# Performance work log

Measured on AMD Instinct MI355X. Metric: run time of the kernel, lower is better.

Reference implementation:

```python
import jax, jax.numpy as jnp
import numpy as np

N = 4096  # number of nodes (matches fill_max of edge indices)


def _dense(edges, n):
    # edges: [2, E] int; dense {0,1} adjacency. Duplicate edges collapse (set semantics).
    return jnp.zeros((n, n), dtype=jnp.float32).at[edges[0], edges[1]].set(1.0)


def setup_inputs() -> dict:
    key = jax.random.key(0)
    ks = jax.random.split(key, 4)
    E = 200000
    mk = lambda k: jax.random.randint(k, (2, E), 0, N, dtype=jnp.int32)
    return {
        "A_pos_t": mk(ks[0]),
        "A_pos_tp1": mk(ks[1]),
        "A_neg_t": mk(ks[2]),
        "A_neg_tp1": mk(ks[3]),
    }


def reference(A_pos_t, A_pos_tp1, A_neg_t, A_neg_tp1):
    p_t = _dense(A_pos_t, N)
    p1 = _dense(A_pos_tp1, N)
    n_t = _dense(A_neg_t, N)
    n1 = _dense(A_neg_tp1, N)

    # edge_index_diff: set symmetric difference == elementwise xor of {0,1} adjacency
    xor_p = p_t + p1 - 2.0 * p_t * p1
    xor_n = n_t + n1 - 2.0 * n_t * n1

    # Balance theory triangle closure on (tp1) graphs.
    # sign(a,b): +1 if pos edge (pos checked first -> priority), -1 elif neg edge.
    sp = p1                      # positive-sign edge indicator
    sn = n1 * (1.0 - p1)         # negative-sign edge indicator (pos has priority)
    off = 1.0 - jnp.eye(N, dtype=jnp.float32)
    spo = sp * off               # exclude b==a / b==c (triples are distinct)
    sno = sn * off

    # number of 2-paths a->b->c with predicted sign +1 / -1
    M_same = spo @ spo + sno @ sno
    M_diff = spo @ sno + sno @ spo

    # the Python loop only infers edges (a,c) with a < c (orientations (i,j,k),(i,k,j),(j,i,k))
    tri = jnp.triu(jnp.ones((N, N), dtype=jnp.float32), k=1)

    ind_p = M_same * tri * (1.0 - p1)  # skip pairs already positively connected
    ind_n = M_diff * tri * (1.0 - n1)  # skip pairs already negatively connected

    # Output: [2, N, N]; entry = xor indicator + indirect-edge multiplicity count
    return jnp.stack([xor_p + ind_p, xor_n + ind_n])
```

## Files before the change

kernel.cpp:

```cpp
#include <hip/hip_runtime.h>


#define NN 4096
#define NW 128
#define MASK_BYTES ((size_t)NN * NW * 4)
#define MASK_WORDS ((size_t)NN * NW)

typedef unsigned int u32;
typedef __attribute__((ext_vector_type(4))) int int4v;
typedef __attribute__((ext_vector_type(4))) float f32x4;

__device__ __forceinline__ void gload_lds16(const char* g, char* l) {
    __builtin_amdgcn_global_load_lds(
        (const __attribute__((address_space(1))) void*)g,
        (__attribute__((address_space(3))) void*)l, 16, 0, 0);
}


__global__ void scatter_all(const int* __restrict__ e0, const int* __restrict__ e1,
                            const int* __restrict__ e2, const int* __restrict__ e3,
                            int E0, int E1, int E2, int E3,
                            u32* __restrict__ ws) {
    int i = blockIdx.x * blockDim.x + threadIdx.x;
    u32* Pt  = ws + 0 * MASK_WORDS;
    u32* P1  = ws + 1 * MASK_WORDS;
    u32* Nt  = ws + 2 * MASK_WORDS;
    u32* N1  = ws + 3 * MASK_WORDS;
    u32* P1T = ws + 4 * MASK_WORDS;
    u32* N1T = ws + 5 * MASK_WORDS;
    if (i < E0) { int r = e0[i], c = e0[i + E0];
        atomicOr(&Pt[r * NW + (c >> 5)], 1u << (c & 31)); }
    if (i < E1) { int r = e1[i], c = e1[i + E1];
        atomicOr(&P1[r * NW + (c >> 5)], 1u << (c & 31));
        atomicOr(&P1T[c * NW + (r >> 5)], 1u << (r & 31)); }
    if (i < E2) { int r = e2[i], c = e2[i + E2];
        atomicOr(&Nt[r * NW + (c >> 5)], 1u << (c & 31)); }
    if (i < E3) { int r = e3[i], c = e3[i + E3];
        atomicOr(&N1[r * NW + (c >> 5)], 1u << (c & 31));
        atomicOr(&N1T[c * NW + (r >> 5)], 1u << (r & 31)); }
}

__device__ __forceinline__ int4v expand_e(u32 sp, u32 sn) {
    int4v E;
    #pragma unroll
    for (int i = 0; i < 4; i++) {
        u32 p = (((sp >> (4 * i)) & 0xFu) * 0x00204081u) & 0x01010101u;
        u32 n = (((sn >> (4 * i)) & 0xFu) * 0x00204081u) & 0x01010101u;
        E[i] = (int)(p | (n << 5));
    }
    return E;
}

__global__ void build_e(const u32* __restrict__ masks,
                        char* __restrict__ E, char* __restrict__ ET) {
    int u = blockIdx.x * blockDim.x + threadIdx.x;
    int half = (u >= (int)MASK_WORDS);
    int wi = half ? u - (int)MASK_WORDS : u;
    const u32* P  = masks + (half ? 4 : 1) * MASK_WORDS;
    const u32* Nm = masks + (half ? 5 : 3) * MASK_WORDS;
    u32 p = P[wi];
    u32 n = Nm[wi] & ~p;
    int a = wi >> 7, col = wi & 127;
    if ((a >> 5) == col) {
        u32 db = 1u << (a & 31);
        p &= ~db; n &= ~db;
    }
    char* dst = (half ? ET : E) + (size_t)a * NN + col * 32;
    *reinterpret_cast<int4v*>(dst)      = expand_e(p & 0xFFFFu, n & 0xFFFFu);
    *reinterpret_cast<int4v*>(dst + 16) = expand_e(p >> 16, n >> 16);
}

__global__ __launch_bounds__(256, 3) void gemm_ep(
    const char* __restrict__ E, const char* __restrict__ ET,
    const u32* __restrict__ Pt, const u32* __restrict__ P1,
    const u32* __restrict__ Nt, const u32* __restrict__ N1,
    float* __restrict__ out)
{
    const int tid = threadIdx.x;
    const size_t plane = (size_t)NN * NN;

    int s_ = ((int)blockIdx.x & 7) * 66 + ((int)blockIdx.x >> 3);
    int by = (int)((65.0f - sqrtf(4225.0f - 8.0f * (float)s_)) * 0.5f);
    if (by > 31) by = 31;
    while (by > 0 && 32 * by - (by * (by - 1)) / 2 > s_) --by;
    while (32 * (by + 1) - ((by + 1) * by) / 2 <= s_) ++by;
    int bx = by + s_ - (32 * by - (by * (by - 1)) / 2);
    const int a0 = by << 7, c0 = bx << 7;

    __shared__ char LB[3][2][8192];

    const int wave = tid >> 6, lane = tid & 63;
    const int wr = (wave >> 1) * 64, wcol = (wave & 1) * 64;
    const int lr = lane & 15, lg = lane >> 4;

    const int rh = tid >> 2, ch = tid & 3;
    const int swz = (ch ^ ((rh >> 1) & 3)) << 4;
    const char* gA = E  + (size_t)(a0 + rh) * NN + swz;
    const char* gB = ET + (size_t)(c0 + rh) * NN + swz;
    const int l16 = tid * 16;

    int4v acc[4][4];
    int4v zero = {0, 0, 0, 0};
    #pragma unroll
    for (int m = 0; m < 4; m++)
        #pragma unroll
        for (int n = 0; n < 4; n++) acc[m][n] = zero;

    #define STAGE(b, t)                                               \
        do {                                                          \
            const int koff = (t) * 64;                                \
            gload_lds16(gA + koff,            &LB[b][0][l16]);        \
            gload_lds16(gA + 64 * NN + koff,  &LB[b][0][4096 + l16]); \
            gload_lds16(gB + koff,            &LB[b][1][l16]);        \
            gload_lds16(gB + 64 * NN + koff,  &LB[b][1][4096 + l16]); \
        } while (0)

    #define COMPUTE(b)                                                         \
        do {                                                                   \
            int4v bf[4];                                                       \
            _Pragma("unroll")                                                  \
            for (int n = 0; n < 4; n++) {                                      \
                int rowb = wcol + n * 16 + lr;                                 \
                bf[n] = *reinterpret_cast<const int4v*>(                       \
                    &LB[b][1][rowb * 64 + ((lg ^ ((rowb >> 1) & 3)) << 4)]);   \
            }                                                                  \
            __builtin_amdgcn_s_setprio(1);                                     \
            _Pragma("unroll")                                                  \
            for (int m = 0; m < 4; m++) {                                      \
                int rowa = wr + m * 16 + lr;                                   \
                int4v af = *reinterpret_cast<const int4v*>(                    \
                    &LB[b][0][rowa * 64 + ((lg ^ ((rowa >> 1) & 3)) << 4)]);   \
                _Pragma("unroll")                                              \
                for (int n = 0; n < 4; n++)                                    \
                    acc[m][n] = __builtin_amdgcn_mfma_i32_16x16x64_i8(         \
                        af, bf[n], acc[m][n], 0, 0, 0);                        \
            }                                                                  \
            __builtin_amdgcn_s_setprio(0);                                     \
        } while (0)

    STAGE(0, 0);
    STAGE(1, 1);
    asm volatile("s_waitcnt vmcnt(4)" ::: "memory");
    __builtin_amdgcn_s_barrier();

    int cur = 0;
    for (int t = 0; t < 62; ++t) {
        int nb = cur + 2; if (nb >= 3) nb -= 3;
        STAGE(nb, t + 2);
        COMPUTE(cur);
        asm volatile("s_waitcnt vmcnt(4)" ::: "memory");
        __builtin_amdgcn_s_barrier();
        cur = (cur == 2) ? 0 : cur + 1;
    }
    COMPUTE(cur);
    asm volatile("s_waitcnt vmcnt(0)" ::: "memory");
    __builtin_amdgcn_s_barrier();
    cur = (cur == 2) ? 0 : cur + 1;
    COMPUTE(cur);
    #undef STAGE
    #undef COMPUTE

    #pragma unroll
    for (int m = 0; m < 4; m++) {
        #pragma unroll
        for (int n = 0; n < 4; n++) {
            #pragma unroll
            for (int q = 0; q < 4; q++) {
                int a = a0 + wr + m * 16 + lg * 4 + q;
                int c = c0 + wcol + n * 16 + lr;
                int widx = a * NW + (c >> 5);
                int bit = c & 31;
                u32 p1 = (P1[widx] >> bit) & 1u;
                u32 n1 = (N1[widx] >> bit) & 1u;
                u32 pt = (Pt[widx] >> bit) & 1u;
                u32 nt = (Nt[widx] >> bit) & 1u;
                int av = acc[m][n][q];
                int Ms = (av & 31) + (av >> 10);
                int Md = (av >> 5) & 31;
                int o0 = (int)(pt ^ p1) + ((a < c && !p1) ? Ms : 0);
                int o1 = (int)(nt ^ n1) + ((a < c && !n1) ? Md : 0);
                size_t oi = (size_t)a * NN + c;
                out[oi] = (float)o0;
                out[plane + oi] = (float)o1;
            }
        }
    }

    if (by != bx) {
        #pragma unroll 4
        for (int pass = 0; pass < 16; ++pass) {
            int e = pass * 1024 + tid * 4;
            int r = e >> 7, cc = e & 127;
            int widx = (c0 + r) * NW + ((a0 + cc) >> 5);
            int sh = cc & 31;
            u32 xp = (P1[widx] ^ Pt[widx]) >> sh;
            u32 xn = (N1[widx] ^ Nt[widx]) >> sh;
            f32x4 o0, o1;
            #pragma unroll
            for (int i = 0; i < 4; i++) {
                o0[i] = (float)((xp >> i) & 1u);
                o1[i] = (float)((xn >> i) & 1u);
            }
            size_t ob = (size_t)(c0 + r) * NN + a0 + cc;
            *reinterpret_cast<f32x4*>(out + ob) = o0;
            *reinterpret_cast<f32x4*>(out + plane + ob) = o1;
        }
    }
}

extern "C" void kernel_launch(void* const* d_in, const int* in_sizes, int n_in,
                              void* d_out, int out_size, void* d_ws, size_t ws_size,
                              hipStream_t stream) {
    char* ws = (char*)d_ws;
    u32* masks = (u32*)ws;
    u32* Pt = masks + 0 * MASK_WORDS;
    u32* P1 = masks + 1 * MASK_WORDS;
    u32* Nt = masks + 2 * MASK_WORDS;
    u32* N1 = masks + 3 * MASK_WORDS;
    char* E  = ws + 6 * MASK_BYTES;
    char* ET = E + (size_t)NN * NN;

    hipMemsetAsync(d_ws, 0, 6 * MASK_BYTES, stream);

    int E0 = in_sizes[0] / 2, E1 = in_sizes[1] / 2;
    int E2 = in_sizes[2] / 2, E3 = in_sizes[3] / 2;
    int Emax = max(max(E0, E1), max(E2, E3));
    scatter_all<<<(Emax + 255) / 256, 256, 0, stream>>>(
        (const int*)d_in[0], (const int*)d_in[1], (const int*)d_in[2],
        (const int*)d_in[3], E0, E1, E2, E3, masks);

    build_e<<<(2 * (int)MASK_WORDS) / 256, 256, 0, stream>>>(masks, E, ET);

    gemm_ep<<<528, 256, 0, stream>>>(E, ET, Pt, P1, Nt, N1, (float*)d_out);
}
```

Before: 150.4 us.

## Fuse scatter, operand build and GEMM into one persistent kernel with grid barriers

Merges the three launches (edge scatter, byte-operand expansion, int8 GEMM with epilogue) into a single 528-block kernel separated by two atomic grid barriers. The transposed bitmasks are no longer scattered with extra atomics; they are built with wave ballots that transpose 32x32 bit tiles. The lower-triangle XOR output writes move before the GEMM phase, and the memset shrinks. This removes launch gaps and half the scatter atomics, but relies on all 528 blocks being co-resident, and the ballot transpose adds ALU work.

```diff
diff --git a/kernel.cpp b/kernel.cpp
--- a/kernel.cpp
+++ b/kernel.cpp
@@ -6,6 +6,10 @@
 #define MASK_BYTES ((size_t)NN * NW * 4)
 #define MASK_WORDS ((size_t)NN * NW)
 
+#define NBLK 528
+#define NTHR 256
+#define GT (NBLK * NTHR)
+
 typedef unsigned int u32;
 typedef __attribute__((ext_vector_type(4))) int int4v;
 typedef __attribute__((ext_vector_type(4))) float f32x4;
@@ -14,30 +18,6 @@
     __builtin_amdgcn_global_load_lds(
         (const __attribute__((address_space(1))) void*)g,
         (__attribute__((address_space(3))) void*)l, 16, 0, 0);
-}
-
-
-__global__ void scatter_all(const int* __restrict__ e0, const int* __restrict__ e1,
-                            const int* __restrict__ e2, const int* __restrict__ e3,
-                            int E0, int E1, int E2, int E3,
-                            u32* __restrict__ ws) {
-    int i = blockIdx.x * blockDim.x + threadIdx.x;
-    u32* Pt  = ws + 0 * MASK_WORDS;
-    u32* P1  = ws + 1 * MASK_WORDS;
-    u32* Nt  = ws + 2 * MASK_WORDS;
-    u32* N1  = ws + 3 * MASK_WORDS;
-    u32* P1T = ws + 4 * MASK_WORDS;
-    u32* N1T = ws + 5 * MASK_WORDS;
-    if (i < E0) { int r = e0[i], c = e0[i + E0];
-        atomicOr(&Pt[r * NW + (c >> 5)], 1u << (c & 31)); }
-    if (i < E1) { int r = e1[i], c = e1[i + E1];
-        atomicOr(&P1[r * NW + (c >> 5)], 1u << (c & 31));
-        atomicOr(&P1T[c * NW + (r >> 5)], 1u << (r & 31)); }
-    if (i < E2) { int r = e2[i], c = e2[i + E2];
-        atomicOr(&Nt[r * NW + (c >> 5)], 1u << (c & 31)); }
-    if (i < E3) { int r = e3[i], c = e3[i + E3];
-        atomicOr(&N1[r * NW + (c >> 5)], 1u << (c & 31));
-        atomicOr(&N1T[c * NW + (r >> 5)], 1u << (r & 31)); }
 }
 
 __device__ __forceinline__ int4v expand_e(u32 sp, u32 sn) {
@@ -51,32 +31,30 @@
     return E;
 }
 
-__global__ void build_e(const u32* __restrict__ masks,
-                        char* __restrict__ E, char* __restrict__ ET) {
-    int u = blockIdx.x * blockDim.x + threadIdx.x;
-    int half = (u >= (int)MASK_WORDS);
-    int wi = half ? u - (int)MASK_WORDS : u;
-    const u32* P  = masks + (half ? 4 : 1) * MASK_WORDS;
-    const u32* Nm = masks + (half ? 5 : 3) * MASK_WORDS;
-    u32 p = P[wi];
-    u32 n = Nm[wi] & ~p;
-    int a = wi >> 7, col = wi & 127;
-    if ((a >> 5) == col) {
-        u32 db = 1u << (a & 31);
-        p &= ~db; n &= ~db;
-    }
-    char* dst = (half ? ET : E) + (size_t)a * NN + col * 32;
-    *reinterpret_cast<int4v*>(dst)      = expand_e(p & 0xFFFFu, n & 0xFFFFu);
-    *reinterpret_cast<int4v*>(dst + 16) = expand_e(p >> 16, n >> 16);
-}
-
-__global__ __launch_bounds__(256, 3) void gemm_ep(
-    const char* __restrict__ E, const char* __restrict__ ET,
-    const u32* __restrict__ Pt, const u32* __restrict__ P1,
-    const u32* __restrict__ Nt, const u32* __restrict__ N1,
-    float* __restrict__ out)
+__device__ __forceinline__ void gridbar(u32* c) {
+    __syncthreads();
+    if (threadIdx.x == 0) {
+        __hip_atomic_fetch_add(c, 1u, __ATOMIC_RELEASE, __HIP_MEMORY_SCOPE_AGENT);
+        while (__hip_atomic_load(c, __ATOMIC_ACQUIRE, __HIP_MEMORY_SCOPE_AGENT)
+               < (u32)NBLK) {}
+    }
+    __syncthreads();
+}
+
+__global__ __launch_bounds__(256, 3) void mega(
+    const int* __restrict__ e0, const int* __restrict__ e1,
+    const int* __restrict__ e2, const int* __restrict__ e3,
+    int E0, int E1, int E2, int E3,
+    u32* __restrict__ masks, u32* __restrict__ bars,
+    char* __restrict__ E, char* __restrict__ ET, float* __restrict__ out)
 {
+    u32* Pt = masks + 0 * MASK_WORDS;
+    u32* P1 = masks + 1 * MASK_WORDS;
+    u32* Nt = masks + 2 * MASK_WORDS;
+    u32* N1 = masks + 3 * MASK_WORDS;
+
     const int tid = threadIdx.x;
+    const int gtid = (int)blockIdx.x * NTHR + tid;
     const size_t plane = (size_t)NN * NN;
 
     int s_ = ((int)blockIdx.x & 7) * 66 + ((int)blockIdx.x >> 3);
@@ -86,6 +64,80 @@
     while (32 * (by + 1) - ((by + 1) * by) / 2 <= s_) ++by;
     int bx = by + s_ - (32 * by - (by * (by - 1)) / 2);
     const int a0 = by << 7, c0 = bx << 7;
+
+    for (int i = gtid; i < E0; i += GT) { int r = e0[i], c = e0[i + E0];
+        atomicOr(&Pt[r * NW + (c >> 5)], 1u << (c & 31)); }
+    for (int i = gtid; i < E1; i += GT) { int r = e1[i], c = e1[i + E1];
+        atomicOr(&P1[r * NW + (c >> 5)], 1u << (c & 31)); }
+    for (int i = gtid; i < E2; i += GT) { int r = e2[i], c = e2[i + E2];
+        atomicOr(&Nt[r * NW + (c >> 5)], 1u << (c & 31)); }
+    for (int i = gtid; i < E3; i += GT) { int r = e3[i], c = e3[i + E3];
+        atomicOr(&N1[r * NW + (c >> 5)], 1u << (c & 31)); }
+    gridbar(&bars[0]);
+
+    if (by != bx) {
+        #pragma unroll 4
+        for (int pass = 0; pass < 16; ++pass) {
+            int e = pass * 1024 + tid * 4;
+            int r = e >> 7, cc = e & 127;
+            int widx = (c0 + r) * NW + ((a0 + cc) >> 5);
+            int sh = cc & 31;
+            u32 xp = (P1[widx] ^ Pt[widx]) >> sh;
+            u32 xn = (N1[widx] ^ Nt[widx]) >> sh;
+            f32x4 o0, o1;
+            #pragma unroll
+            for (int i = 0; i < 4; i++) {
+                o0[i] = (float)((xp >> i) & 1u);
+                o1[i] = (float)((xn >> i) & 1u);
+            }
+            size_t ob = (size_t)(c0 + r) * NN + a0 + cc;
+            *reinterpret_cast<f32x4*>(out + ob) = o0;
+            *reinterpret_cast<f32x4*>(out + plane + ob) = o1;
+        }
+    }
+    for (int w = gtid; w < (int)MASK_WORDS; w += GT) {
+        u32 p = P1[w];
+        u32 n = N1[w] & ~p;
+        int a = w >> 7, col = w & 127;
+        if ((a >> 5) == col) {
+            u32 db = 1u << (a & 31);
+            p &= ~db; n &= ~db;
+        }
+        char* dst = E + (size_t)a * NN + col * 32;
+        *reinterpret_cast<int4v*>(dst)      = expand_e(p & 0xFFFFu, n & 0xFFFFu);
+        *reinterpret_cast<int4v*>(dst + 16) = expand_e(p >> 16, n >> 16);
+    }
+    {
+        int wid = gtid >> 6, lane = tid & 63;
+        for (int t = wid; t < 8192; t += GT / 64) {
+            int ab = t >> 7;
+            int wc = t & 127;
+            u32 pw = P1[(ab * 64 + lane) * NW + wc];
+            u32 nw = N1[(ab * 64 + lane) * NW + wc];
+            u32 myp = 0, myn = 0;
+            #pragma unroll
+            for (int j = 0; j < 32; j++) {
+                unsigned long long bp = __ballot((pw >> j) & 1u);
+                unsigned long long bn = __ballot((nw >> j) & 1u);
+                if ((lane & 31) == j) {
+                    myp = (lane < 32) ? (u32)bp : (u32)(bp >> 32);
+                    myn = (lane < 32) ? (u32)bn : (u32)(bn >> 32);
+                }
+            }
+            u32 p = myp;
+            u32 n = myn & ~p;
+            int c = wc * 32 + (lane & 31);
+            int abase = ab * 64 + (lane >> 5) * 32;
+            if (c >= abase && c < abase + 32) {
+                u32 db = 1u << (c - abase);
+                p &= ~db; n &= ~db;
+            }
+            char* dst = ET + (size_t)c * NN + abase;
+            *reinterpret_cast<int4v*>(dst)      = expand_e(p & 0xFFFFu, n & 0xFFFFu);
+            *reinterpret_cast<int4v*>(dst + 16) = expand_e(p >> 16, n >> 16);
+        }
+    }
+    gridbar(&bars[1]);
 
     __shared__ char LB[3][2][8192];
 
@@ -185,27 +237,6 @@
             }
         }
     }
-
-    if (by != bx) {
-        #pragma unroll 4
-        for (int pass = 0; pass < 16; ++pass) {
-            int e = pass * 1024 + tid * 4;
-            int r = e >> 7, cc = e & 127;
-            int widx = (c0 + r) * NW + ((a0 + cc) >> 5);
-            int sh = cc & 31;
-            u32 xp = (P1[widx] ^ Pt[widx]) >> sh;
-            u32 xn = (N1[widx] ^ Nt[widx]) >> sh;
-            f32x4 o0, o1;
-            #pragma unroll
-            for (int i = 0; i < 4; i++) {
-                o0[i] = (float)((xp >> i) & 1u);
-                o1[i] = (float)((xn >> i) & 1u);
-            }
-            size_t ob = (size_t)(c0 + r) * NN + a0 + cc;
-            *reinterpret_cast<f32x4*>(out + ob) = o0;
-            *reinterpret_cast<f32x4*>(out + plane + ob) = o1;
-        }
-    }
 }
 
 extern "C" void kernel_launch(void* const* d_in, const int* in_sizes, int n_in,
@@ -213,23 +244,19 @@
                               hipStream_t stream) {
     char* ws = (char*)d_ws;
     u32* masks = (u32*)ws;
-    u32* Pt = masks + 0 * MASK_WORDS;
-    u32* P1 = masks + 1 * MASK_WORDS;
-    u32* Nt = masks + 2 * MASK_WORDS;
-    u32* N1 = masks + 3 * MASK_WORDS;
-    char* E  = ws + 6 * MASK_BYTES;
-    char* ET = E + (size_t)NN * NN;
-
-    hipMemsetAsync(d_ws, 0, 6 * MASK_BYTES, stream);
-
+    u32* bars  = (u32*)(ws + 4 * MASK_BYTES);
+    char* Em   = ws + 4 * MASK_BYTES + 4096;
+    char* ETm  = Em + (size_t)NN * NN;
+
+    hipMemsetAsync(d_ws, 0, 4 * MASK_BYTES + 4096, stream);
+
+    const int* e0 = (const int*)d_in[0];
+    const int* e1 = (const int*)d_in[1];
+    const int* e2 = (const int*)d_in[2];
+    const int* e3 = (const int*)d_in[3];
     int E0 = in_sizes[0] / 2, E1 = in_sizes[1] / 2;
     int E2 = in_sizes[2] / 2, E3 = in_sizes[3] / 2;
-    int Emax = max(max(E0, E1), max(E2, E3));
-    scatter_all<<<(Emax + 255) / 256, 256, 0, stream>>>(
-        (const int*)d_in[0], (const int*)d_in[1], (const int*)d_in[2],
-        (const int*)d_in[3], E0, E1, E2, E3, masks);
-
-    build_e<<<(2 * (int)MASK_WORDS) / 256, 256, 0, stream>>>(masks, E, ET);
-
-    gemm_ep<<<528, 256, 0, stream>>>(E, ET, Pt, P1, Nt, N1, (float*)d_out);
-}
+
+    mega<<<NBLK, NTHR, 0, stream>>>(e0, e1, e2, e3, E0, E1, E2, E3,
+                                    masks, bars, Em, ETm, (float*)d_out);
+}
```

Result: slower. 333.7 us (+121.9%).
